# Optimization experiments

Hardware: AMD Instinct MI355X
Metric: run time of the kernel (lower is better)

## Reference

```python
import jax, jax.numpy as jnp
import numpy as np
import math

HEADS = 8
DIM_HEAD = 64
DIM = HEADS * DIM_HEAD  # 512; to_v is Identity so dim must equal heads*dim_head
SCALE = DIM_HEAD ** -0.5


def get_slopes(n):
    def pow2(n):
        start = 2 ** (-2 ** (-(math.log2(n) - 3)))
        return [start * start ** i for i in range(n)]
    if math.log2(n).is_integer():
        return pow2(n)
    c = 2 ** math.floor(math.log2(n))
    return pow2(c) + get_slopes(2 * c)[0::2][: n - c]

SLOPES = jnp.asarray(np.array(get_slopes(HEADS), dtype=np.float32))


def setup_inputs() -> dict:
    key = jax.random.key(0)
    k1, k2, k3, k4 = jax.random.split(key, 4)
    b, n = 4, 2048
    x = jax.random.normal(k1, (b, n, DIM), dtype=jnp.float32)
    # positions: e.g. observation timestamps (days); uniform floats scaled to [0, 365)
    positions = jax.random.uniform(k2, (b, n), dtype=jnp.float32) * 365.0
    Wq = jax.random.normal(k3, (DIM, DIM), dtype=jnp.float32) * (DIM ** -0.5)
    Wk = jax.random.normal(k4, (DIM, DIM), dtype=jnp.float32) * (DIM ** -0.5)
    return {"x": x, "positions": positions, "Wq": Wq, "Wk": Wk}


def reference(x, positions, Wq, Wk):
    b, n, _ = x.shape
    # q, k projections (no bias); v = x (Identity)
    q = (x @ Wq.T).reshape(b, n, HEADS, DIM_HEAD).transpose(0, 2, 1, 3)  # b h n d
    k = (x @ Wk.T).reshape(b, n, HEADS, DIM_HEAD).transpose(0, 2, 1, 3)
    v = x.reshape(b, n, HEADS, DIM_HEAD).transpose(0, 2, 1, 3)
    dots = jnp.einsum('bhid,bhjd->bhij', q, k) * SCALE  # b h n n
    # relative_positions[b,i,j] = -|positions[b,j] - positions[b,i]|
    rel = -jnp.abs(positions[:, None, :] - positions[:, :, None])  # b n n
    alibi = SLOPES[None, :, None, None] * rel[:, None, :, :]  # b h n n
    attn = jax.nn.softmax(dots + alibi, axis=-1)
    out = jnp.einsum('bhij,bhjd->bhid', attn, v)  # b h n d
    return out.transpose(0, 2, 1, 3).reshape(b, n, DIM)
```

## Files before the change

kernel.cpp:

```cpp
#include <hip/hip_runtime.h>
#include <hip/hip_bf16.h>

typedef __bf16 bf16x8 __attribute__((ext_vector_type(8)));
typedef float f32x4 __attribute__((ext_vector_type(4)));
typedef float f32x16 __attribute__((ext_vector_type(16)));

__device__ inline unsigned short f2bf(float f) {
    __hip_bfloat16 h = __float2bfloat16(f);
    return __builtin_bit_cast(unsigned short, h);
}
__device__ inline unsigned cvtpk(float a, float b) {
    unsigned r;
    asm("v_cvt_pk_bf16_f32 %0, %1, %2" : "=v"(r) : "v"(a), "v"(b));
    return r;
}
__device__ inline unsigned pkhi(float lo, float hi) {
    return __builtin_amdgcn_perm(__builtin_bit_cast(unsigned, hi),
                                 __builtin_bit_cast(unsigned, lo), 0x07060302u);
}
__device__ inline float exp2_fast(float x) {
    float r;
    asm("v_exp_f32 %0, %1" : "=v"(r) : "v"(x));
    return r;
}

#define QSCALE 0.1803368801111244f

__global__ __launch_bounds__(256) void gemm_qk(const float* __restrict__ x,
                                               const float* __restrict__ Wq,
                                               const float* __restrict__ Wk,
                                               unsigned short* __restrict__ Qb,
                                               unsigned short* __restrict__ Kb,
                                               unsigned short* __restrict__ Vt) {
    __shared__ __align__(16) unsigned short sA[128 * 40];
    __shared__ __align__(16) unsigned short sB[128 * 40];
    const int tid  = threadIdx.x;
    const int by = blockIdx.y;

    if (by >= 8) {
        const int q = by - 8;
        const int nl = tid & 127, hh = tid >> 7;
        const int h = q * 2 + hh;
        const int g = blockIdx.x * 128 + nl;
        const int b = g >> 11, n = g & 2047;
        const int np = (n & ~15) | (n & 3) | ((n & 4) << 1) | ((n & 8) >> 1);
        const size_t xrow = ((size_t)b * 2048 + n) * 512 + h * 64;
        const size_t vbase = ((size_t)(b * 8 + h) * 64) * 2048 + np;
#pragma unroll
        for (int d0 = 0; d0 < 64; d0 += 4) {
            float4 v = *reinterpret_cast<const float4*>(&x[xrow + d0]);
            Vt[vbase + (size_t)(d0 + 0) * 2048] = f2bf(v.x);
            Vt[vbase + (size_t)(d0 + 1) * 2048] = f2bf(v.y);
            Vt[vbase + (size_t)(d0 + 2) * 2048] = f2bf(v.z);
            Vt[vbase + (size_t)(d0 + 3) * 2048] = f2bf(v.w);
        }
        return;
    }

    const int lane = tid & 63;
    const int wave = tid >> 6;
    const int wr = wave >> 1, wc = wave & 1;
    const int bm = blockIdx.x * 128;
    const float* __restrict__ Bsrc = (by < 4) ? Wq : Wk;
    unsigned short* __restrict__ C = (by < 4) ? Qb : Kb;
    const int bn = (by & 3) * 128;
    const float scale = (by < 4) ? QSCALE : 1.0f;
    const int tr = tid >> 1, th = (tid & 1) * 16;
    const int rl = lane & 15;
    const int kq = (lane >> 4) * 8;

    f32x4 acc[4][4];
#pragma unroll
    for (int m = 0; m < 4; ++m)
#pragma unroll
        for (int n = 0; n < 4; ++n) acc[m][n] = (f32x4){0.f, 0.f, 0.f, 0.f};

    for (int k0 = 0; k0 < 512; k0 += 32) {
        const float* ap = &x[(size_t)(bm + tr) * 512 + k0 + th];
        const float* bp = &Bsrc[(size_t)(bn + tr) * 512 + k0 + th];
        float4 a0 = *reinterpret_cast<const float4*>(ap);
        float4 a1 = *reinterpret_cast<const float4*>(ap + 4);
        float4 a2 = *reinterpret_cast<const float4*>(ap + 8);
        float4 a3 = *reinterpret_cast<const float4*>(ap + 12);
        float4 b0 = *reinterpret_cast<const float4*>(bp);
        float4 b1 = *reinterpret_cast<const float4*>(bp + 4);
        float4 b2 = *reinterpret_cast<const float4*>(bp + 8);
        float4 b3 = *reinterpret_cast<const float4*>(bp + 12);
        uint4 pa0 = {cvtpk(a0.x, a0.y), cvtpk(a0.z, a0.w), cvtpk(a1.x, a1.y), cvtpk(a1.z, a1.w)};
        uint4 pa1 = {cvtpk(a2.x, a2.y), cvtpk(a2.z, a2.w), cvtpk(a3.x, a3.y), cvtpk(a3.z, a3.w)};
        uint4 pb0 = {cvtpk(b0.x, b0.y), cvtpk(b0.z, b0.w), cvtpk(b1.x, b1.y), cvtpk(b1.z, b1.w)};
        uint4 pb1 = {cvtpk(b2.x, b2.y), cvtpk(b2.z, b2.w), cvtpk(b3.x, b3.y), cvtpk(b3.z, b3.w)};
        __syncthreads();
        *reinterpret_cast<uint4*>(&sA[tr * 40 + th])     = pa0;
        *reinterpret_cast<uint4*>(&sA[tr * 40 + th + 8]) = pa1;
        *reinterpret_cast<uint4*>(&sB[tr * 40 + th])     = pb0;
        *reinterpret_cast<uint4*>(&sB[tr * 40 + th + 8]) = pb1;
        __syncthreads();

        bf16x8 af[4], bfv[4];
#pragma unroll
        for (int m = 0; m < 4; ++m)
            af[m] = __builtin_bit_cast(bf16x8,
                *reinterpret_cast<const uint4*>(&sA[(wr * 64 + m * 16 + rl) * 40 + kq]));
#pragma unroll
        for (int n = 0; n < 4; ++n)
            bfv[n] = __builtin_bit_cast(bf16x8,
                *reinterpret_cast<const uint4*>(&sB[(wc * 64 + n * 16 + rl) * 40 + kq]));
#pragma unroll
        for (int m = 0; m < 4; ++m)
#pragma unroll
            for (int n = 0; n < 4; ++n)
                acc[m][n] = __builtin_amdgcn_mfma_f32_16x16x32_bf16(af[m], bfv[n], acc[m][n], 0, 0, 0);
    }

    const int rq = (lane >> 4) * 4;
#pragma unroll
    for (int m = 0; m < 4; ++m) {
        int r = bm + wr * 64 + m * 16 + rq;
#pragma unroll
        for (int n = 0; n < 4; ++n) {
            int c = bn + wc * 64 + n * 16 + rl;
#pragma unroll
            for (int reg = 0; reg < 4; ++reg)
                C[(size_t)(r + reg) * 512 + c] = f2bf(acc[m][n][reg] * scale);
        }
    }
}

__global__ __launch_bounds__(512, 4) void attn_fwd(const unsigned short* __restrict__ Q,
                                                   const unsigned short* __restrict__ Kb,
                                                   const unsigned short* __restrict__ Vt,
                                                   const float* __restrict__ pos,
                                                   float* __restrict__ Out) {
    __shared__ __align__(16) unsigned char smem[42240];
    char* k0b = (char*)smem;
    char* v0b = (char*)smem + 8192;
    char* k1b = (char*)smem + 16384;
    char* v1b = (char*)smem + 24576;
    float* sPosT = (float*)(smem + 32768);
    float* sMl   = (float*)(smem + 40960);

    const int tid  = threadIdx.x;
    const int lane = tid & 63;
    const int w    = tid >> 6;
    const int l31  = lane & 31;
    const int hi   = lane >> 5;
    const int qh   = w & 3;
    const int jp   = w >> 2;
    const int flat = blockIdx.x;
    const int xcd  = flat & 7;
    const int idx  = flat >> 3;
    const int bh   = xcd * 4 + (idx >> 4);
    const int qt   = idx & 15;
    const int b = bh >> 3, h = bh & 7;
    const int q0 = qt * 128 + qh * 32;
    const size_t rowbase = (size_t)b * 2048;
    const int hc = h * 64;
    const float slopeL = ldexpf(1.4426950408889634f, -(h + 1));

    bf16x8 qf0, qf1, qf2, qf3;
    {
        const unsigned short* qp = &Q[(rowbase + q0 + l31) * 512 + hc + hi * 8];
        qf0 = __builtin_bit_cast(bf16x8, *reinterpret_cast<const uint4*>(qp));
        qf1 = __builtin_bit_cast(bf16x8, *reinterpret_cast<const uint4*>(qp + 16));
        qf2 = __builtin_bit_cast(bf16x8, *reinterpret_cast<const uint4*>(qp + 32));
        qf3 = __builtin_bit_cast(bf16x8, *reinterpret_cast<const uint4*>(qp + 48));
    }
    const float ui = slopeL * pos[rowbase + q0 + l31];

    {
        float4 v = reinterpret_cast<const float4*>(pos + rowbase)[tid];
        reinterpret_cast<f32x4*>(sPosT)[tid] =
            (f32x4){v.x * slopeL, v.y * slopeL, v.z * slopeL, v.w * slopeL};
    }

    float lloc = 0.f;
    f32x16 o0, o1;
#pragma unroll
    for (int r = 0; r < 16; ++r) { o0[r] = 0.f; o1[r] = 0.f; }

    const int sr  = tid >> 3;
    const int sce = (tid & 7) * 8;
    const int wbyte = sr * 128 + (((tid & 7) * 16) ^ ((sr & 7) << 4));
    const int kswz = (l31 & 7) << 4;

    uint4 ck, cv;

    auto stage = [&](int j0v) {
        ck = *reinterpret_cast<const uint4*>(&Kb[(rowbase + j0v + sr) * 512 + hc + sce]);
        cv = *reinterpret_cast<const uint4*>(&Vt[((size_t)bh * 64 + sr) * 2048 + j0v + sce]);
    };
    auto writeb = [&](char* KB, char* VB) {
        *reinterpret_cast<uint4*>(KB + wbyte) = ck;
        *reinterpret_cast<uint4*>(VB + wbyte) = cv;
    };
    auto compute = [&](const char* KB, const char* VB, int j0) {
        const char* kr = KB + (32 * jp + l31) * 128;
        f32x16 s;
#pragma unroll
        for (int r = 0; r < 16; ++r) s[r] = 0.f;
        __builtin_amdgcn_s_setprio(1);
#pragma unroll
        for (int ks = 0; ks < 4; ++ks) {
            bf16x8 kf = __builtin_bit_cast(bf16x8,
                *reinterpret_cast<const uint4*>(kr + ((ks * 32 + hi * 16) ^ kswz)));
            bf16x8 qq = (ks == 0) ? qf0 : (ks == 1) ? qf1 : (ks == 2) ? qf2 : qf3;
            s = __builtin_amdgcn_mfma_f32_32x32x16_bf16(kf, qq, s, 0, 0, 0);
        }
        __builtin_amdgcn_s_setprio(0);

        float ls = 0.f;
#pragma unroll
        for (int t = 0; t < 4; ++t) {
            f32x4 u = *reinterpret_cast<const f32x4*>(&sPosT[j0 + 32 * jp + 8 * t + 4 * hi]);
#pragma unroll
            for (int r = 0; r < 4; ++r) {
                float p = exp2_fast(s[4 * t + r] - fabsf(u[r] - ui));
                s[4 * t + r] = p;
                ls += p;
            }
        }
        lloc += ls;

        bf16x8 pf0 = __builtin_bit_cast(bf16x8, (uint4){
            pkhi(s[0], s[1]),  pkhi(s[2], s[3]),   pkhi(s[4], s[5]),   pkhi(s[6], s[7])});
        bf16x8 pf1 = __builtin_bit_cast(bf16x8, (uint4){
            pkhi(s[8], s[9]),  pkhi(s[10], s[11]), pkhi(s[12], s[13]), pkhi(s[14], s[15])});

        const char* vr0 = VB + l31 * 128;
        const char* vr1 = VB + (32 + l31) * 128;
        __builtin_amdgcn_s_setprio(1);
#pragma unroll
        for (int ks = 0; ks < 2; ++ks) {
            const int cb = (64 * jp + ks * 32 + hi * 16) ^ kswz;
            bf16x8 v0 = __builtin_bit_cast(bf16x8, *reinterpret_cast<const uint4*>(vr0 + cb));
            bf16x8 v1 = __builtin_bit_cast(bf16x8, *reinterpret_cast<const uint4*>(vr1 + cb));
            bf16x8 pf = ks ? pf1 : pf0;
            o0 = __builtin_amdgcn_mfma_f32_32x32x16_bf16(v0, pf, o0, 0, 0, 0);
            o1 = __builtin_amdgcn_mfma_f32_32x32x16_bf16(v1, pf, o1, 0, 0, 0);
        }
        __builtin_amdgcn_s_setprio(0);
    };

    stage(0);
    writeb(k0b, v0b);
    stage(64);
    __syncthreads();

    for (int t = 0; t < 32; t += 2) {
        writeb(k1b, v1b);
        if (t + 2 < 32) stage((t + 2) * 64);
        compute(k0b, v0b, t * 64);
        __syncthreads();
        if (t + 2 < 32) {
            writeb(k0b, v0b);
            if (t + 3 < 32) stage((t + 3) * 64);
        }
        compute(k1b, v1b, (t + 1) * 64);
        __syncthreads();
    }

    float lt = lloc + __shfl_xor(lloc, 32, 64);
    float* sM = (float*)smem;
    const int key = (lane & 7) << 2;
    if (jp == 1) {
        float* dst = sM + qh * 2048 + lane * 32;
#pragma unroll
        for (int i = 0; i < 4; ++i) {
            f32x4 t0 = {o0[4 * i], o0[4 * i + 1], o0[4 * i + 2], o0[4 * i + 3]};
            f32x4 t1 = {o1[4 * i], o1[4 * i + 1], o1[4 * i + 2], o1[4 * i + 3]};
            *reinterpret_cast<f32x4*>(dst + ((4 * i) ^ key))      = t0;
            *reinterpret_cast<f32x4*>(dst + ((16 + 4 * i) ^ key)) = t1;
        }
        sMl[qh * 64 + lane] = lt;
    }
    __syncthreads();
    if (jp == 0) {
        const float* src = sM + qh * 2048 + lane * 32;
#pragma unroll
        for (int i = 0; i < 4; ++i) {
            f32x4 t0 = *reinterpret_cast<const f32x4*>(src + ((4 * i) ^ key));
            f32x4 t1 = *reinterpret_cast<const f32x4*>(src + ((16 + 4 * i) ^ key));
#pragma unroll
            for (int r = 0; r < 4; ++r) { o0[4 * i + r] += t0[r]; o1[4 * i + r] += t1[r]; }
        }
        const float linv = 1.0f / (lt + sMl[qh * 64 + lane]);
        float* orow = &Out[(rowbase + q0 + l31) * 512 + hc];
#pragma unroll
        for (int t = 0; t < 4; ++t) {
            f32x4 a, c;
#pragma unroll
            for (int r = 0; r < 4; ++r) {
                a[r] = o0[4 * t + r] * linv;
                c[r] = o1[4 * t + r] * linv;
            }
            *reinterpret_cast<f32x4*>(orow + 8 * t + 4 * hi)      = a;
            *reinterpret_cast<f32x4*>(orow + 32 + 8 * t + 4 * hi) = c;
        }
    }
}

extern "C" void kernel_launch(void* const* d_in, const int* in_sizes, int n_in,
                              void* d_out, int out_size, void* d_ws, size_t ws_size,
                              hipStream_t stream) {
    const float* x   = (const float*)d_in[0];
    const float* pos = (const float*)d_in[1];
    const float* Wq  = (const float*)d_in[2];
    const float* Wk  = (const float*)d_in[3];
    float* out = (float*)d_out;

    unsigned short* Qb  = (unsigned short*)d_ws;
    unsigned short* Kbf = Qb  + 4194304;
    unsigned short* Vtb = Kbf + 4194304;

    gemm_qk<<<dim3(64, 12), dim3(256), 0, stream>>>(x, Wq, Wk, Qb, Kbf, Vtb);
    attn_fwd<<<dim3(512), dim3(512), 0, stream>>>(Qb, Kbf, Vtb, pos, out);
}
```

Before: 75.15 us.

## Pre-convert x and weights to bf16 in a separate prep kernel before GEMM

```diff
diff --git a/kernel.cpp b/kernel.cpp
--- a/kernel.cpp
+++ b/kernel.cpp
@@ -26,23 +26,39 @@
 
 #define QSCALE 0.1803368801111244f
 
-__global__ __launch_bounds__(256) void gemm_qk(const float* __restrict__ x,
-                                               const float* __restrict__ Wq,
-                                               const float* __restrict__ Wk,
-                                               unsigned short* __restrict__ Qb,
-                                               unsigned short* __restrict__ Kb,
-                                               unsigned short* __restrict__ Vt) {
-    __shared__ __align__(16) unsigned short sA[128 * 40];
-    __shared__ __align__(16) unsigned short sB[128 * 40];
-    const int tid  = threadIdx.x;
-    const int by = blockIdx.y;
-
-    if (by >= 8) {
-        const int q = by - 8;
-        const int nl = tid & 127, hh = tid >> 7;
-        const int h = q * 2 + hh;
-        const int g = blockIdx.x * 128 + nl;
-        const int b = g >> 11, n = g & 2047;
+__global__ __launch_bounds__(256) void prep(const float* __restrict__ x,
+                                            const float* __restrict__ Wq,
+                                            const float* __restrict__ Wk,
+                                            unsigned short* __restrict__ xb,
+                                            unsigned short* __restrict__ wqb,
+                                            unsigned short* __restrict__ wkb,
+                                            unsigned short* __restrict__ Vt) {
+    const int blk = blockIdx.x;
+    const int tid = threadIdx.x;
+    if (blk < 2048) {
+        const size_t i = ((size_t)blk * 256 + tid) * 8;
+        float4 v0 = *reinterpret_cast<const float4*>(x + i);
+        float4 v1 = *reinterpret_cast<const float4*>(x + i + 4);
+        uint4 o = {cvtpk(v0.x, v0.y), cvtpk(v0.z, v0.w), cvtpk(v1.x, v1.y), cvtpk(v1.z, v1.w)};
+        *reinterpret_cast<uint4*>(xb + i) = o;
+    } else if (blk < 2176) {
+        const size_t i = ((size_t)(blk - 2048) * 256 + tid) * 8;
+        float4 v0 = *reinterpret_cast<const float4*>(Wq + i);
+        float4 v1 = *reinterpret_cast<const float4*>(Wq + i + 4);
+        uint4 o = {cvtpk(v0.x * QSCALE, v0.y * QSCALE), cvtpk(v0.z * QSCALE, v0.w * QSCALE),
+                   cvtpk(v1.x * QSCALE, v1.y * QSCALE), cvtpk(v1.z * QSCALE, v1.w * QSCALE)};
+        *reinterpret_cast<uint4*>(wqb + i) = o;
+    } else if (blk < 2304) {
+        const size_t i = ((size_t)(blk - 2176) * 256 + tid) * 8;
+        float4 v0 = *reinterpret_cast<const float4*>(Wk + i);
+        float4 v1 = *reinterpret_cast<const float4*>(Wk + i + 4);
+        uint4 o = {cvtpk(v0.x, v0.y), cvtpk(v0.z, v0.w), cvtpk(v1.x, v1.y), cvtpk(v1.z, v1.w)};
+        *reinterpret_cast<uint4*>(wkb + i) = o;
+    } else {
+        const int idx = blk - 2304;
+        const int lane = tid & 63, w = tid >> 6;
+        const int bx = idx & 7, h = (idx >> 3) & 7, b = idx >> 6;
+        const int n = bx * 256 + w * 64 + lane;
         const int np = (n & ~15) | (n & 3) | ((n & 4) << 1) | ((n & 8) >> 1);
         const size_t xrow = ((size_t)b * 2048 + n) * 512 + h * 64;
         const size_t vbase = ((size_t)(b * 8 + h) * 64) * 2048 + np;
@@ -54,17 +70,25 @@
             Vt[vbase + (size_t)(d0 + 2) * 2048] = f2bf(v.z);
             Vt[vbase + (size_t)(d0 + 3) * 2048] = f2bf(v.w);
         }
-        return;
-    }
-
+    }
+}
+
+__global__ __launch_bounds__(256) void gemm_qk(const unsigned short* __restrict__ xb,
+                                               const unsigned short* __restrict__ wqb,
+                                               const unsigned short* __restrict__ wkb,
+                                               unsigned short* __restrict__ Qb,
+                                               unsigned short* __restrict__ Kb) {
+    __shared__ __align__(16) unsigned short sA[128 * 40];
+    __shared__ __align__(16) unsigned short sB[128 * 40];
+    const int tid  = threadIdx.x;
+    const int by   = blockIdx.y;
     const int lane = tid & 63;
     const int wave = tid >> 6;
     const int wr = wave >> 1, wc = wave & 1;
     const int bm = blockIdx.x * 128;
-    const float* __restrict__ Bsrc = (by < 4) ? Wq : Wk;
+    const unsigned short* __restrict__ Bsrc = (by < 4) ? wqb : wkb;
     unsigned short* __restrict__ C = (by < 4) ? Qb : Kb;
     const int bn = (by & 3) * 128;
-    const float scale = (by < 4) ? QSCALE : 1.0f;
     const int tr = tid >> 1, th = (tid & 1) * 16;
     const int rl = lane & 15;
     const int kq = (lane >> 4) * 8;
@@ -76,25 +100,17 @@
         for (int n = 0; n < 4; ++n) acc[m][n] = (f32x4){0.f, 0.f, 0.f, 0.f};
 
     for (int k0 = 0; k0 < 512; k0 += 32) {
-        const float* ap = &x[(size_t)(bm + tr) * 512 + k0 + th];
-        const float* bp = &Bsrc[(size_t)(bn + tr) * 512 + k0 + th];
-        float4 a0 = *reinterpret_cast<const float4*>(ap);
-        float4 a1 = *reinterpret_cast<const float4*>(ap + 4);
-        float4 a2 = *reinterpret_cast<const float4*>(ap + 8);
-        float4 a3 = *reinterpret_cast<const float4*>(ap + 12);
-        float4 b0 = *reinterpret_cast<const float4*>(bp);
-        float4 b1 = *reinterpret_cast<const float4*>(bp + 4);
-        float4 b2 = *reinterpret_cast<const float4*>(bp + 8);
-        float4 b3 = *reinterpret_cast<const float4*>(bp + 12);
-        uint4 pa0 = {cvtpk(a0.x, a0.y), cvtpk(a0.z, a0.w), cvtpk(a1.x, a1.y), cvtpk(a1.z, a1.w)};
-        uint4 pa1 = {cvtpk(a2.x, a2.y), cvtpk(a2.z, a2.w), cvtpk(a3.x, a3.y), cvtpk(a3.z, a3.w)};
-        uint4 pb0 = {cvtpk(b0.x, b0.y), cvtpk(b0.z, b0.w), cvtpk(b1.x, b1.y), cvtpk(b1.z, b1.w)};
-        uint4 pb1 = {cvtpk(b2.x, b2.y), cvtpk(b2.z, b2.w), cvtpk(b3.x, b3.y), cvtpk(b3.z, b3.w)};
+        const unsigned short* ap = &xb[(size_t)(bm + tr) * 512 + k0 + th];
+        const unsigned short* bp = &Bsrc[(size_t)(bn + tr) * 512 + k0 + th];
+        uint4 a0 = *reinterpret_cast<const uint4*>(ap);
+        uint4 a1 = *reinterpret_cast<const uint4*>(ap + 8);
+        uint4 b0 = *reinterpret_cast<const uint4*>(bp);
+        uint4 b1 = *reinterpret_cast<const uint4*>(bp + 8);
         __syncthreads();
-        *reinterpret_cast<uint4*>(&sA[tr * 40 + th])     = pa0;
-        *reinterpret_cast<uint4*>(&sA[tr * 40 + th + 8]) = pa1;
-        *reinterpret_cast<uint4*>(&sB[tr * 40 + th])     = pb0;
-        *reinterpret_cast<uint4*>(&sB[tr * 40 + th + 8]) = pb1;
+        *reinterpret_cast<uint4*>(&sA[tr * 40 + th])     = a0;
+        *reinterpret_cast<uint4*>(&sA[tr * 40 + th + 8]) = a1;
+        *reinterpret_cast<uint4*>(&sB[tr * 40 + th])     = b0;
+        *reinterpret_cast<uint4*>(&sB[tr * 40 + th + 8]) = b1;
         __syncthreads();
 
         bf16x8 af[4], bfv[4];
@@ -122,7 +138,7 @@
             int c = bn + wc * 64 + n * 16 + rl;
 #pragma unroll
             for (int reg = 0; reg < 4; ++reg)
-                C[(size_t)(r + reg) * 512 + c] = f2bf(acc[m][n][reg] * scale);
+                C[(size_t)(r + reg) * 512 + c] = f2bf(acc[m][n][reg]);
         }
     }
 }
@@ -309,10 +325,14 @@
     const float* Wk  = (const float*)d_in[3];
     float* out = (float*)d_out;
 
-    unsigned short* Qb  = (unsigned short*)d_ws;
+    unsigned short* xb  = (unsigned short*)d_ws;
+    unsigned short* wqb = xb  + 4194304;
+    unsigned short* wkb = wqb + 262144;
+    unsigned short* Qb  = wkb + 262144;
     unsigned short* Kbf = Qb  + 4194304;
     unsigned short* Vtb = Kbf + 4194304;
 
-    gemm_qk<<<dim3(64, 12), dim3(256), 0, stream>>>(x, Wq, Wk, Qb, Kbf, Vtb);
+    prep<<<dim3(2560), dim3(256), 0, stream>>>(x, Wq, Wk, xb, wqb, wkb, Vtb);
+    gemm_qk<<<dim3(64, 8), dim3(256), 0, stream>>>(xb, wqb, wkb, Qb, Kbf);
     attn_fwd<<<dim3(512), dim3(512), 0, stream>>>(Qb, Kbf, Vtb, pos, out);
 }
```

Result: slower. 84.61 us (+12.6%).
